# Optimization experiments

Measured on AMD Instinct MI355X. Metric: run time of the kernel, lower is better.

Reference implementation:

```python
import jax, jax.numpy as jnp
import numpy as np

# Approximate EMD matching (Fan et al. approxmatch): 10 annealed soft-assignment
# rounds with levels -4^j for j = 7..-1 and level 0 for the final round.
_LEVELS = jnp.asarray([-(4.0 ** j) for j in range(7, -2, -1)] + [0.0], dtype=jnp.float32)


def _approx_match(d2, n, m):
    # d2: [b, n, m] squared pairwise distances
    b = d2.shape[0]
    factorl = max(n, m) / float(n)
    factorr = max(n, m) / float(m)
    remainl0 = jnp.full((b, n), factorl, dtype=d2.dtype)
    remainr0 = jnp.full((b, m), factorr, dtype=d2.dtype)
    match0 = jnp.zeros_like(d2)

    def step(carry, level):
        match, remainl, remainr = carry
        w = jnp.exp(level * d2) * remainr[:, None, :]            # [b,n,m]
        w = w / (jnp.sum(w, axis=-1, keepdims=True) + 1e-9)      # row-normalize
        w = w * remainl[:, :, None]                              # scale by left capacity
        ss2 = jnp.sum(w, axis=1)                                 # [b,m] column mass
        s = jnp.minimum(remainr / (ss2 + 1e-9), 1.0)             # column saturation
        w = w * s[:, None, :]
        match = match + w
        remainl = jnp.maximum(remainl - jnp.sum(w, axis=-1), 0.0)
        remainr = jnp.maximum(remainr - jnp.sum(w, axis=1), 0.0)
        return (match, remainl, remainr), None

    (match, _, _), _ = jax.lax.scan(step, (match0, remainl0, remainr0), _LEVELS)
    return match


def setup_inputs() -> dict:
    key = jax.random.key(0)
    k1, k2 = jax.random.split(key)
    xyz1 = jax.random.normal(k1, (16, 2048, 3), dtype=jnp.float32)
    xyz2 = jax.random.normal(k2, (16, 2048, 3), dtype=jnp.float32)
    return {"xyz1": xyz1, "xyz2": xyz2}


def reference(xyz1, xyz2):
    n, m = xyz1.shape[1], xyz2.shape[1]
    diff = xyz1[:, :, None, :] - xyz2[:, None, :, :]             # [b,n,m,3]
    d2 = jnp.sum(diff * diff, axis=-1)                           # [b,n,m]
    match = _approx_match(d2, n, m)
    dist = jnp.sqrt(jnp.maximum(d2, 1e-12))
    cost = jnp.sum(match * dist, axis=(1, 2))                    # [b]
    return cost
```

## Files before the change

kernel.cpp:

```cpp
#include <hip/hip_runtime.h>
#include <math.h>

#define B 16
#define N 2048
#define M 2048
#define BN (B * N)
#define LOG2E 1.4426950408889634f

#define CJ 128
#define NCH (M / CJ)
#define TPB 128
#define RPT 4
#define RBLK (TPB * RPT)

typedef float v2f __attribute__((ext_vector_type(2)));

#define EXP2F(x) __builtin_amdgcn_exp2f(x)
#define SQRTF(x) __builtin_amdgcn_sqrtf(x)

__device__ inline v2f exp2v(v2f a) {
    v2f r;
    r.x = EXP2F(a.x);
    r.y = EXP2F(a.y);
    return r;
}

__global__ __launch_bounds__(256) void k_pack(const float* __restrict__ xyz1,
                                              const float* __restrict__ xyz2,
                                              float4* __restrict__ p1,
                                              float4* __restrict__ p2) {
    int idx = blockIdx.x * 256 + threadIdx.x;
    const float* s = (idx < BN) ? (xyz1 + 3 * (size_t)idx)
                                : (xyz2 + 3 * (size_t)(idx - BN));
    float x = s[0], y = s[1], z = s[2];
    float n = fmaf(x, x, fmaf(y, y, z * z));
    float4 v = make_float4(x, y, z, n);
    if (idx < BN) p1[idx] = v;
    else p2[idx - BN] = v;
}

__global__ __launch_bounds__(256) void k_init(float* __restrict__ rl0,
                                              float* __restrict__ rr0,
                                              float* __restrict__ rs0,
                                              float* __restrict__ rs2,
                                              float* __restrict__ t1b,
                                              float* __restrict__ ss20,
                                              float* __restrict__ cost) {
    int idx = blockIdx.x * 256 + threadIdx.x;
    rl0[idx] = 1.0f;
    rr0[idx] = 1.0f;
    rs0[idx] = 0.0f;
    rs2[idx] = 0.0f;
    t1b[idx] = 0.0f;
    ss20[idx] = 0.0f;
    if (idx < B) cost[idx] = 0.0f;
}

__global__ __launch_bounds__(TPB, 2) void k_rowsum0(const float4* __restrict__ p1,
                                                    const float4* __restrict__ p2,
                                                    float* __restrict__ rs,
                                                    float c2) {
    __shared__ float4 tile4[CJ];
    const int b = blockIdx.z;
    const int tx = threadIdx.x;
    const int i0 = blockIdx.y * RBLK + tx;

    {
        int gj = b * M + blockIdx.x * CJ + tx;
        float4 f = p2[gj];
        tile4[tx] = make_float4(f.x, f.y, f.z, c2 * f.w);
    }
    __syncthreads();

    float4 fa = p1[b * N + i0];
    float4 fb = p1[b * N + i0 + TPB];
    float4 fc = p1[b * N + i0 + 2 * TPB];
    float4 fd = p1[b * N + i0 + 3 * TPB];
    const float m2c = -2.0f * c2;
    v2f Xp0 = {m2c * fa.x, m2c * fb.x}, Xp1 = {m2c * fc.x, m2c * fd.x};
    v2f Yp0 = {m2c * fa.y, m2c * fb.y}, Yp1 = {m2c * fc.y, m2c * fd.y};
    v2f Zp0 = {m2c * fa.z, m2c * fb.z}, Zp1 = {m2c * fc.z, m2c * fd.z};
    v2f ni0 = {c2 * fa.w, c2 * fb.w}, ni1 = {c2 * fc.w, c2 * fd.w};

    v2f acc0 = {0.0f, 0.0f}, acc1 = {0.0f, 0.0f};
#pragma unroll 8
    for (int t = 0; t < CJ; ++t) {
        float4 q4 = tile4[t];
        v2f arg0 = q4.x * Xp0 + (q4.y * Yp0 + (q4.z * Zp0 + (ni0 + q4.w)));
        v2f arg1 = q4.x * Xp1 + (q4.y * Yp1 + (q4.z * Zp1 + (ni1 + q4.w)));
        acc0 += exp2v(arg0);
        acc1 += exp2v(arg1);
    }
    atomicAdd(&rs[b * N + i0], acc0.x);
    atomicAdd(&rs[b * N + i0 + TPB], acc0.y);
    atomicAdd(&rs[b * N + i0 + 2 * TPB], acc1.x);
    atomicAdd(&rs[b * N + i0 + 3 * TPB], acc1.y);
}

__global__ __launch_bounds__(TPB, 2) void k_colsum(const float4* __restrict__ p1,
                                                   const float4* __restrict__ p2,
                                                   const float* __restrict__ rl_in,
                                                   float* __restrict__ rl_out,
                                                   const float* __restrict__ rs_prev,
                                                   const float* __restrict__ rs_cur,
                                                   float* __restrict__ rs_zero,
                                                   const float* __restrict__ t1_in,
                                                   float* __restrict__ t1_zero,
                                                   const float* __restrict__ rr,
                                                   float* __restrict__ ss2_acc,
                                                   float cS) {
    __shared__ float4 tile4[CJ];
    __shared__ float tileA[CJ];
    const int b = blockIdx.z;
    const int tx = threadIdx.x;
    const int j0 = blockIdx.y * RBLK + tx;

    {
        int gi = b * N + blockIdx.x * CJ + tx;
        float4 f = p1[gi];
        float rlo = rl_in[gi];
        float ap = rlo / (rs_prev[gi] + 1e-9f);
        float rln = fmaxf(rlo - ap * t1_in[gi], 0.0f);
        float a = rln / (rs_cur[gi] + 1e-9f);
        tile4[tx] = make_float4(f.x, f.y, f.z, cS * f.w);
        tileA[tx] = a;
        if (blockIdx.y == 0) {
            rl_out[gi] = rln;
            t1_zero[gi] = 0.0f;
            rs_zero[gi] = 0.0f;
        }
    }
    __syncthreads();

    float4 fa = p2[b * M + j0];
    float4 fb = p2[b * M + j0 + TPB];
    float4 fc = p2[b * M + j0 + 2 * TPB];
    float4 fd = p2[b * M + j0 + 3 * TPB];
    const float m2c = -2.0f * cS;
    v2f Xp0 = {m2c * fa.x, m2c * fb.x}, Xp1 = {m2c * fc.x, m2c * fd.x};
    v2f Yp0 = {m2c * fa.y, m2c * fb.y}, Yp1 = {m2c * fc.y, m2c * fd.y};
    v2f Zp0 = {m2c * fa.z, m2c * fb.z}, Zp1 = {m2c * fc.z, m2c * fd.z};
    v2f nj0 = {cS * fa.w, cS * fb.w}, nj1 = {cS * fc.w, cS * fd.w};

    v2f acc0 = {0.0f, 0.0f}, acc1 = {0.0f, 0.0f};
#pragma unroll 8
    for (int t = 0; t < CJ; ++t) {
        float4 q4 = tile4[t];
        float av = tileA[t];
        v2f arg0 = q4.x * Xp0 + (q4.y * Yp0 + (q4.z * Zp0 + (nj0 + q4.w)));
        v2f arg1 = q4.x * Xp1 + (q4.y * Yp1 + (q4.z * Zp1 + (nj1 + q4.w)));
        acc0 += exp2v(arg0) * av;
        acc1 += exp2v(arg1) * av;
    }
    atomicAdd(&ss2_acc[b * M + j0], acc0.x * rr[b * M + j0]);
    atomicAdd(&ss2_acc[b * M + j0 + TPB], acc0.y * rr[b * M + j0 + TPB]);
    atomicAdd(&ss2_acc[b * M + j0 + 2 * TPB], acc1.x * rr[b * M + j0 + 2 * TPB]);
    atomicAdd(&ss2_acc[b * M + j0 + 3 * TPB], acc1.y * rr[b * M + j0 + 3 * TPB]);
}

__global__ __launch_bounds__(256) void k_suma(const float* __restrict__ rl_in,
                                              float* __restrict__ rl_out,
                                              const float* __restrict__ rs_prev,
                                              const float* __restrict__ rs_cur,
                                              const float* __restrict__ t1_in,
                                              float* __restrict__ S) {
    __shared__ float red[4];
    const int b = blockIdx.x;
    const int tx = threadIdx.x;
    float s = 0.0f;
#pragma unroll
    for (int k = 0; k < N / 256; ++k) {
        int gi = b * N + k * 256 + tx;
        float rlo = rl_in[gi];
        float ap = rlo / (rs_prev[gi] + 1e-9f);
        float rln = fmaxf(rlo - ap * t1_in[gi], 0.0f);
        rl_out[gi] = rln;
        s += rln / (rs_cur[gi] + 1e-9f);
    }
#pragma unroll
    for (int off = 32; off > 0; off >>= 1)
        s += __shfl_down(s, off, 64);
    if ((tx & 63) == 0) red[tx >> 6] = s;
    __syncthreads();
    if (tx == 0) S[b] = red[0] + red[1] + red[2] + red[3];
}

__global__ __launch_bounds__(256) void k_mulss2(const float* __restrict__ rr,
                                                const float* __restrict__ S,
                                                float* __restrict__ ss2_out) {
    int idx = blockIdx.x * 256 + threadIdx.x;
    ss2_out[idx] = rr[idx] * S[idx >> 11];
}

template <int MODE>
__global__ __launch_bounds__(TPB, 2) void k_fused(const float4* __restrict__ p1,
                                                  const float4* __restrict__ p2,
                                                  const float* __restrict__ rr_in,
                                                  float* __restrict__ rr_out,
                                                  const float* __restrict__ ss2_in,
                                                  float* __restrict__ ss2_zero,
                                                  const float* __restrict__ rl_new,
                                                  const float* __restrict__ rs_cur,
                                                  float* __restrict__ rs_next,
                                                  float* __restrict__ t1_acc,
                                                  float* __restrict__ cost,
                                                  float cS, float invS) {
    __shared__ float4 tile4[CJ];
    __shared__ float2 tile2[CJ];
    const int b = blockIdx.z;
    const int tx = threadIdx.x;
    const int i0 = blockIdx.y * RBLK + tx;

    {
        int gj = b * M + blockIdx.x * CJ + tx;
        float4 f = p2[gj];
        float rrv = rr_in[gj];
        float sv = ss2_in[gj];
        float s = fminf(rrv / (sv + 1e-9f), 1.0f);
        float q = rrv * s;
        float rrn = fmaxf(rrv - sv * s, 0.0f);
        tile4[tx] = make_float4(f.x, f.y, f.z, q);
        tile2[tx] = make_float2(rrn, cS * f.w);
        if (MODE != 2 && blockIdx.y == 0) {
            rr_out[gj] = rrn;
            ss2_zero[gj] = 0.0f;
        }
    }
    __syncthreads();

    float4 fa = p1[b * N + i0];
    float4 fb = p1[b * N + i0 + TPB];
    float4 fc = p1[b * N + i0 + 2 * TPB];
    float4 fd = p1[b * N + i0 + 3 * TPB];
    const float m2c = -2.0f * cS;
    v2f Xp0 = {m2c * fa.x, m2c * fb.x}, Xp1 = {m2c * fc.x, m2c * fd.x};
    v2f Yp0 = {m2c * fa.y, m2c * fb.y}, Yp1 = {m2c * fc.y, m2c * fd.y};
    v2f Zp0 = {m2c * fa.z, m2c * fb.z}, Zp1 = {m2c * fc.z, m2c * fd.z};
    v2f ni0 = {cS * fa.w, cS * fb.w}, ni1 = {cS * fc.w, cS * fd.w};

    v2f T10 = {0.0f, 0.0f}, T20 = {0.0f, 0.0f}, rs0v = {0.0f, 0.0f};
    v2f T11 = {0.0f, 0.0f}, T21 = {0.0f, 0.0f}, rs1v = {0.0f, 0.0f};
#pragma unroll 8
    for (int t = 0; t < CJ; ++t) {
        float4 q4 = tile4[t];
        float2 rn = tile2[t];
        v2f arg0 = q4.x * Xp0 + (q4.y * Yp0 + (q4.z * Zp0 + (ni0 + rn.y)));
        v2f arg1 = q4.x * Xp1 + (q4.y * Yp1 + (q4.z * Zp1 + (ni1 + rn.y)));
        v2f el0, el1, en0, en1;
        if (MODE == 0) {
            en0 = exp2v(arg0);
            en1 = exp2v(arg1);
            v2f e20 = en0 * en0, e21 = en1 * en1;
            el0 = e20 * e20;
            el1 = e21 * e21;
        } else if (MODE == 1) {
            el0 = exp2v(arg0);
            el1 = exp2v(arg1);
        }
        v2f d20 = arg0 * invS, d21 = arg1 * invS;
        d20.x = fmaxf(d20.x, 1e-12f);
        d20.y = fmaxf(d20.y, 1e-12f);
        d21.x = fmaxf(d21.x, 1e-12f);
        d21.y = fmaxf(d21.y, 1e-12f);
        v2f sd0, sd1;
        sd0.x = SQRTF(d20.x);
        sd0.y = SQRTF(d20.y);
        sd1.x = SQRTF(d21.x);
        sd1.y = SQRTF(d21.y);
        v2f wq0, wq1;
        if (MODE == 2) {
            wq0.x = q4.w; wq0.y = q4.w;
            wq1.x = q4.w; wq1.y = q4.w;
        } else {
            wq0 = el0 * q4.w;
            wq1 = el1 * q4.w;
        }
        T10 += wq0;
        T11 += wq1;
        T20 += wq0 * sd0;
        T21 += wq1 * sd1;
        if (MODE == 0) {
            rs0v += en0 * rn.x;
            rs1v += en1 * rn.x;
        } else if (MODE == 1) {
            rs0v += rn.x;
            rs1v += rn.x;
        }
    }

    const int gi0 = b * N + i0;
    if (MODE != 2) {
        atomicAdd(&t1_acc[gi0], T10.x);
        atomicAdd(&t1_acc[gi0 + TPB], T10.y);
        atomicAdd(&t1_acc[gi0 + 2 * TPB], T11.x);
        atomicAdd(&t1_acc[gi0 + 3 * TPB], T11.y);
        atomicAdd(&rs_next[gi0], rs0v.x);
        atomicAdd(&rs_next[gi0 + TPB], rs0v.y);
        atomicAdd(&rs_next[gi0 + 2 * TPB], rs1v.x);
        atomicAdd(&rs_next[gi0 + 3 * TPB], rs1v.y);
    }

    float aa = rl_new[gi0] / (rs_cur[gi0] + 1e-9f);
    float ab = rl_new[gi0 + TPB] / (rs_cur[gi0 + TPB] + 1e-9f);
    float ac = rl_new[gi0 + 2 * TPB] / (rs_cur[gi0 + 2 * TPB] + 1e-9f);
    float ad = rl_new[gi0 + 3 * TPB] / (rs_cur[gi0 + 3 * TPB] + 1e-9f);
    float contrib = fmaf(aa, T20.x, fmaf(ab, T20.y, fmaf(ac, T21.x, ad * T21.y)));
#pragma unroll
    for (int off = 32; off > 0; off >>= 1)
        contrib += __shfl_down(contrib, off, 64);
    if ((threadIdx.x & 63) == 0) atomicAdd(&cost[b], contrib);
}

extern "C" void kernel_launch(void* const* d_in, const int* in_sizes, int n_in,
                              void* d_out, int out_size, void* d_ws, size_t ws_size,
                              hipStream_t stream) {
    const float* xyz1 = (const float*)d_in[0];
    const float* xyz2 = (const float*)d_in[1];
    float* cost = (float*)d_out;

    float* ws = (float*)d_ws;
    float* rl[2] = {ws + 0 * BN, ws + 1 * BN};
    float* rr[2] = {ws + 2 * BN, ws + 3 * BN};
    float* rs[3] = {ws + 4 * BN, ws + 5 * BN, ws + 6 * BN};
    float* ss2b[2] = {ws + 7 * BN, ws + 8 * BN};
    float* t1[2] = {ws + 9 * BN, ws + 10 * BN};
    float4* p1 = (float4*)(ws + 11 * BN);
    float4* p2 = (float4*)(ws + 15 * BN);
    float* S = ws + 19 * BN;

    static const float levels[10] = {-16384.0f, -4096.0f, -1024.0f, -256.0f,
                                     -64.0f,    -16.0f,   -4.0f,    -1.0f,
                                     -0.25f,    0.0f};
    float c2[10];
    for (int l = 0; l < 10; ++l) c2[l] = levels[l] * LOG2E;

    dim3 grid(NCH, N / RBLK, B);
    dim3 blk(TPB);

    k_pack<<<dim3(2 * BN / 256), dim3(256), 0, stream>>>(xyz1, xyz2, p1, p2);
    k_init<<<dim3(BN / 256), dim3(256), 0, stream>>>(rl[0], rr[0], rs[0], rs[2],
                                                     t1[1], ss2b[0], cost);
    k_rowsum0<<<grid, blk, 0, stream>>>(p1, p2, rs[0], c2[0]);

    for (int l = 0; l < 10; ++l) {
        int p = l & 1;
        if (l < 9) {
            k_colsum<<<grid, blk, 0, stream>>>(
                p1, p2, rl[p], rl[1 - p], rs[(l + 2) % 3], rs[l % 3],
                rs[(l + 1) % 3], t1[1 - p], t1[p], rr[p], ss2b[p], c2[l]);
        } else {
            k_suma<<<dim3(B), dim3(256), 0, stream>>>(
                rl[p], rl[1 - p], rs[(l + 2) % 3], rs[l % 3], t1[1 - p], S);
            k_mulss2<<<dim3(BN / 256), dim3(256), 0, stream>>>(rr[p], S, ss2b[p]);
        }

        if (l <= 7) {
            float cS = c2[l + 1];
            k_fused<0><<<grid, blk, 0, stream>>>(
                p1, p2, rr[p], rr[1 - p], ss2b[p], ss2b[1 - p], rl[1 - p],
                rs[l % 3], rs[(l + 1) % 3], t1[p], cost, cS, 1.0f / cS);
        } else if (l == 8) {
            float cS = c2[8];
            k_fused<1><<<grid, blk, 0, stream>>>(
                p1, p2, rr[p], rr[1 - p], ss2b[p], ss2b[1 - p], rl[1 - p],
                rs[l % 3], rs[(l + 1) % 3], t1[p], cost, cS, 1.0f / cS);
        } else {
            k_fused<2><<<grid, blk, 0, stream>>>(
                p1, p2, rr[p], rr[1 - p], ss2b[p], ss2b[1 - p], rl[1 - p],
                rs[l % 3], rs[(l + 1) % 3], t1[p], cost, 1.0f, 1.0f);
        }
    }
}
```

Before: 609.1 us.

## Read column tiles directly from global memory instead of staging in LDS

```diff
diff --git a/kernel.cpp b/kernel.cpp
--- a/kernel.cpp
+++ b/kernel.cpp
@@ -28,15 +28,21 @@
 __global__ __launch_bounds__(256) void k_pack(const float* __restrict__ xyz1,
                                               const float* __restrict__ xyz2,
                                               float4* __restrict__ p1,
-                                              float4* __restrict__ p2) {
+                                              float4* __restrict__ p2,
+                                              float4* __restrict__ p2s,
+                                              float c20) {
     int idx = blockIdx.x * 256 + threadIdx.x;
     const float* s = (idx < BN) ? (xyz1 + 3 * (size_t)idx)
                                 : (xyz2 + 3 * (size_t)(idx - BN));
     float x = s[0], y = s[1], z = s[2];
     float n = fmaf(x, x, fmaf(y, y, z * z));
     float4 v = make_float4(x, y, z, n);
-    if (idx < BN) p1[idx] = v;
-    else p2[idx - BN] = v;
+    if (idx < BN) {
+        p1[idx] = v;
+    } else {
+        p2[idx - BN] = v;
+        p2s[idx - BN] = make_float4(x, y, z, c20 * n);
+    }
 }
 
 __global__ __launch_bounds__(256) void k_init(float* __restrict__ rl0,
@@ -57,20 +63,13 @@
 }
 
 __global__ __launch_bounds__(TPB, 2) void k_rowsum0(const float4* __restrict__ p1,
-                                                    const float4* __restrict__ p2,
+                                                    const float4* __restrict__ p2s,
                                                     float* __restrict__ rs,
                                                     float c2) {
-    __shared__ float4 tile4[CJ];
     const int b = blockIdx.z;
     const int tx = threadIdx.x;
     const int i0 = blockIdx.y * RBLK + tx;
-
-    {
-        int gj = b * M + blockIdx.x * CJ + tx;
-        float4 f = p2[gj];
-        tile4[tx] = make_float4(f.x, f.y, f.z, c2 * f.w);
-    }
-    __syncthreads();
+    const float4* __restrict__ g = p2s + b * M + blockIdx.x * CJ;
 
     float4 fa = p1[b * N + i0];
     float4 fb = p1[b * N + i0 + TPB];
@@ -85,7 +84,7 @@
     v2f acc0 = {0.0f, 0.0f}, acc1 = {0.0f, 0.0f};
 #pragma unroll 8
     for (int t = 0; t < CJ; ++t) {
-        float4 q4 = tile4[t];
+        float4 q4 = g[t];
         v2f arg0 = q4.x * Xp0 + (q4.y * Yp0 + (q4.z * Zp0 + (ni0 + q4.w)));
         v2f arg1 = q4.x * Xp1 + (q4.y * Yp1 + (q4.z * Zp1 + (ni1 + q4.w)));
         acc0 += exp2v(arg0);
@@ -109,8 +108,7 @@
                                                    const float* __restrict__ rr,
                                                    float* __restrict__ ss2_acc,
                                                    float cS) {
-    __shared__ float4 tile4[CJ];
-    __shared__ float tileA[CJ];
+    __shared__ float2 tileC[CJ];
     const int b = blockIdx.z;
     const int tx = threadIdx.x;
     const int j0 = blockIdx.y * RBLK + tx;
@@ -122,8 +120,7 @@
         float ap = rlo / (rs_prev[gi] + 1e-9f);
         float rln = fmaxf(rlo - ap * t1_in[gi], 0.0f);
         float a = rln / (rs_cur[gi] + 1e-9f);
-        tile4[tx] = make_float4(f.x, f.y, f.z, cS * f.w);
-        tileA[tx] = a;
+        tileC[tx] = make_float2(a, cS * f.w);
         if (blockIdx.y == 0) {
             rl_out[gi] = rln;
             t1_zero[gi] = 0.0f;
@@ -131,6 +128,8 @@
         }
     }
     __syncthreads();
+
+    const float4* __restrict__ g = p1 + b * N + blockIdx.x * CJ;
 
     float4 fa = p2[b * M + j0];
     float4 fb = p2[b * M + j0 + TPB];
@@ -145,12 +144,12 @@
     v2f acc0 = {0.0f, 0.0f}, acc1 = {0.0f, 0.0f};
 #pragma unroll 8
     for (int t = 0; t < CJ; ++t) {
-        float4 q4 = tile4[t];
-        float av = tileA[t];
-        v2f arg0 = q4.x * Xp0 + (q4.y * Yp0 + (q4.z * Zp0 + (nj0 + q4.w)));
-        v2f arg1 = q4.x * Xp1 + (q4.y * Yp1 + (q4.z * Zp1 + (nj1 + q4.w)));
-        acc0 += exp2v(arg0) * av;
-        acc1 += exp2v(arg1) * av;
+        float4 q4 = g[t];
+        float2 cv = tileC[t];
+        v2f arg0 = q4.x * Xp0 + (q4.y * Yp0 + (q4.z * Zp0 + (nj0 + cv.y)));
+        v2f arg1 = q4.x * Xp1 + (q4.y * Yp1 + (q4.z * Zp1 + (nj1 + cv.y)));
+        acc0 += exp2v(arg0) * cv.x;
+        acc1 += exp2v(arg1) * cv.x;
     }
     atomicAdd(&ss2_acc[b * M + j0], acc0.x * rr[b * M + j0]);
     atomicAdd(&ss2_acc[b * M + j0 + TPB], acc0.y * rr[b * M + j0 + TPB]);
@@ -192,41 +191,40 @@
     ss2_out[idx] = rr[idx] * S[idx >> 11];
 }
 
+__global__ __launch_bounds__(256) void k_prepf(const float4* __restrict__ p2,
+                                               const float* __restrict__ rr_in,
+                                               float* __restrict__ rr_out,
+                                               const float* __restrict__ ss2_in,
+                                               float* __restrict__ ss2_zero,
+                                               float4* __restrict__ F4,
+                                               float cS) {
+    int j = blockIdx.x * 256 + threadIdx.x;
+    float4 f = p2[j];
+    float rrv = rr_in[j];
+    float sv = ss2_in[j];
+    float s = fminf(rrv / (sv + 1e-9f), 1.0f);
+    float q = rrv * s;
+    float rrn = fmaxf(rrv - sv * s, 0.0f);
+    F4[j] = make_float4(q, rrn, cS * f.w, 0.0f);
+    rr_out[j] = rrn;
+    ss2_zero[j] = 0.0f;
+}
+
 template <int MODE>
 __global__ __launch_bounds__(TPB, 2) void k_fused(const float4* __restrict__ p1,
                                                   const float4* __restrict__ p2,
-                                                  const float* __restrict__ rr_in,
-                                                  float* __restrict__ rr_out,
-                                                  const float* __restrict__ ss2_in,
-                                                  float* __restrict__ ss2_zero,
+                                                  const float4* __restrict__ F4,
                                                   const float* __restrict__ rl_new,
                                                   const float* __restrict__ rs_cur,
                                                   float* __restrict__ rs_next,
                                                   float* __restrict__ t1_acc,
                                                   float* __restrict__ cost,
                                                   float cS, float invS) {
-    __shared__ float4 tile4[CJ];
-    __shared__ float2 tile2[CJ];
     const int b = blockIdx.z;
     const int tx = threadIdx.x;
     const int i0 = blockIdx.y * RBLK + tx;
-
-    {
-        int gj = b * M + blockIdx.x * CJ + tx;
-        float4 f = p2[gj];
-        float rrv = rr_in[gj];
-        float sv = ss2_in[gj];
-        float s = fminf(rrv / (sv + 1e-9f), 1.0f);
-        float q = rrv * s;
-        float rrn = fmaxf(rrv - sv * s, 0.0f);
-        tile4[tx] = make_float4(f.x, f.y, f.z, q);
-        tile2[tx] = make_float2(rrn, cS * f.w);
-        if (MODE != 2 && blockIdx.y == 0) {
-            rr_out[gj] = rrn;
-            ss2_zero[gj] = 0.0f;
-        }
-    }
-    __syncthreads();
+    const float4* __restrict__ g = p2 + b * M + blockIdx.x * CJ;
+    const float4* __restrict__ h = F4 + b * M + blockIdx.x * CJ;
 
     float4 fa = p1[b * N + i0];
     float4 fb = p1[b * N + i0 + TPB];
@@ -242,10 +240,10 @@
     v2f T11 = {0.0f, 0.0f}, T21 = {0.0f, 0.0f}, rs1v = {0.0f, 0.0f};
 #pragma unroll 8
     for (int t = 0; t < CJ; ++t) {
-        float4 q4 = tile4[t];
-        float2 rn = tile2[t];
-        v2f arg0 = q4.x * Xp0 + (q4.y * Yp0 + (q4.z * Zp0 + (ni0 + rn.y)));
-        v2f arg1 = q4.x * Xp1 + (q4.y * Yp1 + (q4.z * Zp1 + (ni1 + rn.y)));
+        float4 q4 = g[t];
+        float4 f4 = h[t];
+        v2f arg0 = q4.x * Xp0 + (q4.y * Yp0 + (q4.z * Zp0 + (ni0 + f4.z)));
+        v2f arg1 = q4.x * Xp1 + (q4.y * Yp1 + (q4.z * Zp1 + (ni1 + f4.z)));
         v2f el0, el1, en0, en1;
         if (MODE == 0) {
             en0 = exp2v(arg0);
@@ -269,22 +267,22 @@
         sd1.y = SQRTF(d21.y);
         v2f wq0, wq1;
         if (MODE == 2) {
-            wq0.x = q4.w; wq0.y = q4.w;
-            wq1.x = q4.w; wq1.y = q4.w;
+            wq0.x = f4.x; wq0.y = f4.x;
+            wq1.x = f4.x; wq1.y = f4.x;
         } else {
-            wq0 = el0 * q4.w;
-            wq1 = el1 * q4.w;
+            wq0 = el0 * f4.x;
+            wq1 = el1 * f4.x;
         }
         T10 += wq0;
         T11 += wq1;
         T20 += wq0 * sd0;
         T21 += wq1 * sd1;
         if (MODE == 0) {
-            rs0v += en0 * rn.x;
-            rs1v += en1 * rn.x;
+            rs0v += en0 * f4.y;
+            rs1v += en1 * f4.y;
         } else if (MODE == 1) {
-            rs0v += rn.x;
-            rs1v += rn.x;
+            rs0v += f4.y;
+            rs1v += f4.y;
         }
     }
 
@@ -326,7 +324,9 @@
     float* t1[2] = {ws + 9 * BN, ws + 10 * BN};
     float4* p1 = (float4*)(ws + 11 * BN);
     float4* p2 = (float4*)(ws + 15 * BN);
-    float* S = ws + 19 * BN;
+    float4* p2s = (float4*)(ws + 19 * BN);
+    float4* F4 = (float4*)(ws + 23 * BN);
+    float* S = ws + 27 * BN;
 
     static const float levels[10] = {-16384.0f, -4096.0f, -1024.0f, -256.0f,
                                      -64.0f,    -16.0f,   -4.0f,    -1.0f,
@@ -337,10 +337,11 @@
     dim3 grid(NCH, N / RBLK, B);
     dim3 blk(TPB);
 
-    k_pack<<<dim3(2 * BN / 256), dim3(256), 0, stream>>>(xyz1, xyz2, p1, p2);
+    k_pack<<<dim3(2 * BN / 256), dim3(256), 0, stream>>>(xyz1, xyz2, p1, p2,
+                                                         p2s, c2[0]);
     k_init<<<dim3(BN / 256), dim3(256), 0, stream>>>(rl[0], rr[0], rs[0], rs[2],
                                                      t1[1], ss2b[0], cost);
-    k_rowsum0<<<grid, blk, 0, stream>>>(p1, p2, rs[0], c2[0]);
+    k_rowsum0<<<grid, blk, 0, stream>>>(p1, p2s, rs[0], c2[0]);
 
     for (int l = 0; l < 10; ++l) {
         int p = l & 1;
@@ -354,20 +355,24 @@
             k_mulss2<<<dim3(BN / 256), dim3(256), 0, stream>>>(rr[p], S, ss2b[p]);
         }
 
+        float cS = (l <= 7) ? c2[l + 1] : ((l == 8) ? c2[8] : 1.0f);
+        float invS = (l <= 8) ? (1.0f / cS) : 1.0f;
+
+        k_prepf<<<dim3(BN / 256), dim3(256), 0, stream>>>(
+            p2, rr[p], rr[1 - p], ss2b[p], ss2b[1 - p], F4, cS);
+
         if (l <= 7) {
-            float cS = c2[l + 1];
-            k_fused<0><<<grid, blk, 0, stream>>>(
-                p1, p2, rr[p], rr[1 - p], ss2b[p], ss2b[1 - p], rl[1 - p],
-                rs[l % 3], rs[(l + 1) % 3], t1[p], cost, cS, 1.0f / cS);
+            k_fused<0><<<grid, blk, 0, stream>>>(p1, p2, F4, rl[1 - p],
+                                                 rs[l % 3], rs[(l + 1) % 3],
+                                                 t1[p], cost, cS, invS);
         } else if (l == 8) {
-            float cS = c2[8];
-            k_fused<1><<<grid, blk, 0, stream>>>(
-                p1, p2, rr[p], rr[1 - p], ss2b[p], ss2b[1 - p], rl[1 - p],
-                rs[l % 3], rs[(l + 1) % 3], t1[p], cost, cS, 1.0f / cS);
+            k_fused<1><<<grid, blk, 0, stream>>>(p1, p2, F4, rl[1 - p],
+                                                 rs[l % 3], rs[(l + 1) % 3],
+                                                 t1[p], cost, cS, invS);
         } else {
-            k_fused<2><<<grid, blk, 0, stream>>>(
-                p1, p2, rr[p], rr[1 - p], ss2b[p], ss2b[1 - p], rl[1 - p],
-                rs[l % 3], rs[(l + 1) % 3], t1[p], cost, 1.0f, 1.0f);
-        }
-    }
-}
+            k_fused<2><<<grid, blk, 0, stream>>>(p1, p2, F4, rl[1 - p],
+                                                 rs[l % 3], rs[(l + 1) % 3],
+                                                 t1[p], cost, cS, invS);
+        }
+    }
+}
```

After: 626.3 us. 1.03x slower.

## Replace atomic accumulation with per-chunk partial buffers and separate reduction kernels

Applied to the files above, without the earlier changes.

```diff
diff --git a/kernel.cpp b/kernel.cpp
--- a/kernel.cpp
+++ b/kernel.cpp
@@ -44,7 +44,6 @@
                                               float* __restrict__ rs0,
                                               float* __restrict__ rs2,
                                               float* __restrict__ t1b,
-                                              float* __restrict__ ss20,
                                               float* __restrict__ cost) {
     int idx = blockIdx.x * 256 + threadIdx.x;
     rl0[idx] = 1.0f;
@@ -52,13 +51,36 @@
     rs0[idx] = 0.0f;
     rs2[idx] = 0.0f;
     t1b[idx] = 0.0f;
-    ss20[idx] = 0.0f;
     if (idx < B) cost[idx] = 0.0f;
+}
+
+__global__ __launch_bounds__(256) void k_reduce_rs(const float* __restrict__ rp,
+                                                   float* __restrict__ rs_out) {
+    int i = blockIdx.x * 256 + threadIdx.x;
+    float s = 0.0f;
+#pragma unroll
+    for (int k = 0; k < NCH; ++k) s += rp[k * BN + i];
+    rs_out[i] = s;
+}
+
+__global__ __launch_bounds__(256) void k_reduce2(const float* __restrict__ tp,
+                                                 float* __restrict__ t1_out,
+                                                 const float* __restrict__ rp,
+                                                 float* __restrict__ rs_out) {
+    int i = blockIdx.x * 256 + threadIdx.x;
+    float s = 0.0f, t = 0.0f;
+#pragma unroll
+    for (int k = 0; k < NCH; ++k) {
+        t += tp[k * BN + i];
+        s += rp[k * BN + i];
+    }
+    t1_out[i] = t;
+    rs_out[i] = s;
 }
 
 __global__ __launch_bounds__(TPB, 2) void k_rowsum0(const float4* __restrict__ p1,
                                                     const float4* __restrict__ p2,
-                                                    float* __restrict__ rs,
+                                                    float* __restrict__ rsp,
                                                     float c2) {
     __shared__ float4 tile4[CJ];
     const int b = blockIdx.z;
@@ -91,10 +113,11 @@
         acc0 += exp2v(arg0);
         acc1 += exp2v(arg1);
     }
-    atomicAdd(&rs[b * N + i0], acc0.x);
-    atomicAdd(&rs[b * N + i0 + TPB], acc0.y);
-    atomicAdd(&rs[b * N + i0 + 2 * TPB], acc1.x);
-    atomicAdd(&rs[b * N + i0 + 3 * TPB], acc1.y);
+    const int pb = blockIdx.x * BN + b * N + i0;
+    rsp[pb] = acc0.x;
+    rsp[pb + TPB] = acc0.y;
+    rsp[pb + 2 * TPB] = acc1.x;
+    rsp[pb + 3 * TPB] = acc1.y;
 }
 
 __global__ __launch_bounds__(TPB, 2) void k_colsum(const float4* __restrict__ p1,
@@ -103,11 +126,9 @@
                                                    float* __restrict__ rl_out,
                                                    const float* __restrict__ rs_prev,
                                                    const float* __restrict__ rs_cur,
-                                                   float* __restrict__ rs_zero,
                                                    const float* __restrict__ t1_in,
-                                                   float* __restrict__ t1_zero,
                                                    const float* __restrict__ rr,
-                                                   float* __restrict__ ss2_acc,
+                                                   float* __restrict__ ss2p,
                                                    float cS) {
     __shared__ float4 tile4[CJ];
     __shared__ float tileA[CJ];
@@ -124,11 +145,7 @@
         float a = rln / (rs_cur[gi] + 1e-9f);
         tile4[tx] = make_float4(f.x, f.y, f.z, cS * f.w);
         tileA[tx] = a;
-        if (blockIdx.y == 0) {
-            rl_out[gi] = rln;
-            t1_zero[gi] = 0.0f;
-            rs_zero[gi] = 0.0f;
-        }
+        if (blockIdx.y == 0) rl_out[gi] = rln;
     }
     __syncthreads();
 
@@ -152,10 +169,12 @@
         acc0 += exp2v(arg0) * av;
         acc1 += exp2v(arg1) * av;
     }
-    atomicAdd(&ss2_acc[b * M + j0], acc0.x * rr[b * M + j0]);
-    atomicAdd(&ss2_acc[b * M + j0 + TPB], acc0.y * rr[b * M + j0 + TPB]);
-    atomicAdd(&ss2_acc[b * M + j0 + 2 * TPB], acc1.x * rr[b * M + j0 + 2 * TPB]);
-    atomicAdd(&ss2_acc[b * M + j0 + 3 * TPB], acc1.y * rr[b * M + j0 + 3 * TPB]);
+    const int gj = b * M + j0;
+    const int pb = blockIdx.x * BN + gj;
+    ss2p[pb] = acc0.x * rr[gj];
+    ss2p[pb + TPB] = acc0.y * rr[gj + TPB];
+    ss2p[pb + 2 * TPB] = acc1.x * rr[gj + 2 * TPB];
+    ss2p[pb + 3 * TPB] = acc1.y * rr[gj + 3 * TPB];
 }
 
 __global__ __launch_bounds__(256) void k_suma(const float* __restrict__ rl_in,
@@ -198,11 +217,10 @@
                                                   const float* __restrict__ rr_in,
                                                   float* __restrict__ rr_out,
                                                   const float* __restrict__ ss2_in,
-                                                  float* __restrict__ ss2_zero,
                                                   const float* __restrict__ rl_new,
                                                   const float* __restrict__ rs_cur,
-                                                  float* __restrict__ rs_next,
-                                                  float* __restrict__ t1_acc,
+                                                  float* __restrict__ rsp,
+                                                  float* __restrict__ t1p,
                                                   float* __restrict__ cost,
                                                   float cS, float invS) {
     __shared__ float4 tile4[CJ];
@@ -215,16 +233,20 @@
         int gj = b * M + blockIdx.x * CJ + tx;
         float4 f = p2[gj];
         float rrv = rr_in[gj];
-        float sv = ss2_in[gj];
+        float sv;
+        if (MODE == 2) {
+            sv = ss2_in[gj];
+        } else {
+            sv = 0.0f;
+#pragma unroll
+            for (int k = 0; k < NCH; ++k) sv += ss2_in[k * BN + gj];
+        }
         float s = fminf(rrv / (sv + 1e-9f), 1.0f);
         float q = rrv * s;
         float rrn = fmaxf(rrv - sv * s, 0.0f);
         tile4[tx] = make_float4(f.x, f.y, f.z, q);
         tile2[tx] = make_float2(rrn, cS * f.w);
-        if (MODE != 2 && blockIdx.y == 0) {
-            rr_out[gj] = rrn;
-            ss2_zero[gj] = 0.0f;
-        }
+        if (MODE != 2 && blockIdx.y == 0) rr_out[gj] = rrn;
     }
     __syncthreads();
 
@@ -290,14 +312,15 @@
 
     const int gi0 = b * N + i0;
     if (MODE != 2) {
-        atomicAdd(&t1_acc[gi0], T10.x);
-        atomicAdd(&t1_acc[gi0 + TPB], T10.y);
-        atomicAdd(&t1_acc[gi0 + 2 * TPB], T11.x);
-        atomicAdd(&t1_acc[gi0 + 3 * TPB], T11.y);
-        atomicAdd(&rs_next[gi0], rs0v.x);
-        atomicAdd(&rs_next[gi0 + TPB], rs0v.y);
-        atomicAdd(&rs_next[gi0 + 2 * TPB], rs1v.x);
-        atomicAdd(&rs_next[gi0 + 3 * TPB], rs1v.y);
+        const int pb = blockIdx.x * BN + gi0;
+        t1p[pb] = T10.x;
+        t1p[pb + TPB] = T10.y;
+        t1p[pb + 2 * TPB] = T11.x;
+        t1p[pb + 3 * TPB] = T11.y;
+        rsp[pb] = rs0v.x;
+        rsp[pb + TPB] = rs0v.y;
+        rsp[pb + 2 * TPB] = rs1v.x;
+        rsp[pb + 3 * TPB] = rs1v.y;
     }
 
     float aa = rl_new[gi0] / (rs_cur[gi0] + 1e-9f);
@@ -322,11 +345,14 @@
     float* rl[2] = {ws + 0 * BN, ws + 1 * BN};
     float* rr[2] = {ws + 2 * BN, ws + 3 * BN};
     float* rs[3] = {ws + 4 * BN, ws + 5 * BN, ws + 6 * BN};
-    float* ss2b[2] = {ws + 7 * BN, ws + 8 * BN};
-    float* t1[2] = {ws + 9 * BN, ws + 10 * BN};
-    float4* p1 = (float4*)(ws + 11 * BN);
-    float4* p2 = (float4*)(ws + 15 * BN);
-    float* S = ws + 19 * BN;
+    float* t1[2] = {ws + 7 * BN, ws + 8 * BN};
+    float* ss2d = ws + 9 * BN;
+    float4* p1 = (float4*)(ws + 10 * BN);
+    float4* p2 = (float4*)(ws + 14 * BN);
+    float* S = ws + 18 * BN;
+    float* t1p = ws + 18 * BN + 64;
+    float* rsp = t1p + (size_t)NCH * BN;
+    float* ss2p = rsp + (size_t)NCH * BN;
 
     static const float levels[10] = {-16384.0f, -4096.0f, -1024.0f, -256.0f,
                                      -64.0f,    -16.0f,   -4.0f,    -1.0f,
@@ -336,38 +362,44 @@
 
     dim3 grid(NCH, N / RBLK, B);
     dim3 blk(TPB);
-
-    k_pack<<<dim3(2 * BN / 256), dim3(256), 0, stream>>>(xyz1, xyz2, p1, p2);
-    k_init<<<dim3(BN / 256), dim3(256), 0, stream>>>(rl[0], rr[0], rs[0], rs[2],
-                                                     t1[1], ss2b[0], cost);
-    k_rowsum0<<<grid, blk, 0, stream>>>(p1, p2, rs[0], c2[0]);
+    dim3 rgrid(BN / 256), rblk(256);
+
+    k_pack<<<dim3(2 * BN / 256), rblk, 0, stream>>>(xyz1, xyz2, p1, p2);
+    k_init<<<rgrid, rblk, 0, stream>>>(rl[0], rr[0], rs[0], rs[2], t1[1], cost);
+    k_rowsum0<<<grid, blk, 0, stream>>>(p1, p2, rsp, c2[0]);
+    k_reduce_rs<<<rgrid, rblk, 0, stream>>>(rsp, rs[0]);
 
     for (int l = 0; l < 10; ++l) {
         int p = l & 1;
         if (l < 9) {
             k_colsum<<<grid, blk, 0, stream>>>(
                 p1, p2, rl[p], rl[1 - p], rs[(l + 2) % 3], rs[l % 3],
-                rs[(l + 1) % 3], t1[1 - p], t1[p], rr[p], ss2b[p], c2[l]);
+                t1[1 - p], rr[p], ss2p, c2[l]);
         } else {
-            k_suma<<<dim3(B), dim3(256), 0, stream>>>(
+            k_suma<<<dim3(B), rblk, 0, stream>>>(
                 rl[p], rl[1 - p], rs[(l + 2) % 3], rs[l % 3], t1[1 - p], S);
-            k_mulss2<<<dim3(BN / 256), dim3(256), 0, stream>>>(rr[p], S, ss2b[p]);
+            k_mulss2<<<rgrid, rblk, 0, stream>>>(rr[p], S, ss2d);
         }
 
         if (l <= 7) {
             float cS = c2[l + 1];
             k_fused<0><<<grid, blk, 0, stream>>>(
-                p1, p2, rr[p], rr[1 - p], ss2b[p], ss2b[1 - p], rl[1 - p],
-                rs[l % 3], rs[(l + 1) % 3], t1[p], cost, cS, 1.0f / cS);
+                p1, p2, rr[p], rr[1 - p], ss2p, rl[1 - p], rs[l % 3],
+                rsp, t1p, cost, cS, 1.0f / cS);
         } else if (l == 8) {
             float cS = c2[8];
             k_fused<1><<<grid, blk, 0, stream>>>(
-                p1, p2, rr[p], rr[1 - p], ss2b[p], ss2b[1 - p], rl[1 - p],
-                rs[l % 3], rs[(l + 1) % 3], t1[p], cost, cS, 1.0f / cS);
+                p1, p2, rr[p], rr[1 - p], ss2p, rl[1 - p], rs[l % 3],
+                rsp, t1p, cost, cS, 1.0f / cS);
         } else {
             k_fused<2><<<grid, blk, 0, stream>>>(
-                p1, p2, rr[p], rr[1 - p], ss2b[p], ss2b[1 - p], rl[1 - p],
-                rs[l % 3], rs[(l + 1) % 3], t1[p], cost, 1.0f, 1.0f);
-        }
-    }
-}
+                p1, p2, rr[p], rr[1 - p], ss2d, rl[1 - p], rs[l % 3],
+                rsp, t1p, cost, 1.0f, 1.0f);
+        }
+
+        if (l <= 8) {
+            k_reduce2<<<rgrid, rblk, 0, stream>>>(t1p, t1[p], rsp,
+                                                  rs[(l + 1) % 3]);
+        }
+    }
+}
```

After: 616.9 us. About the same (+1.3%).
